# Performance work log

Measured on AMD Instinct MI355X. Metric: run time of the kernel, lower is better.

The kernel has to match this reference:

```python
import jax, jax.numpy as jnp
import numpy as np
from jax import lax

B, C, H, W = 16, 512, 32, 32
CQ = C // 8  # 64
EPS = 1e-5
NEG_SLOPE = 0.2


def _conv1x1(x, Wm, b):
    # x: [B,C,H,W], Wm: [O,C] (1x1 conv kernel squeezed), b: [O]
    return jnp.einsum('oc,bchw->bohw', Wm, x) + b[None, :, None, None]


def _calc_mean_std(feat):
    b, c = feat.shape[:2]
    v = feat.reshape(b, c, -1)
    mean = v.mean(axis=2)[:, :, None, None]
    var = v.var(axis=2, ddof=1) + EPS  # torch .var is unbiased
    std = jnp.sqrt(var)[:, :, None, None]
    return mean, std


def setup_inputs() -> dict:
    key = jax.random.key(0)
    ks = jax.random.split(key, 8)
    s = 0.02
    return {
        'inp': jax.random.normal(ks[0], (B, C, H, W), jnp.float32),
        'x': jax.random.normal(ks[1], (B, C, H, W), jnp.float32),
        'y': jax.random.normal(ks[2], (B, C, H, W), jnp.float32),
        'Wq': jax.random.normal(ks[3], (CQ, C), jnp.float32) * s,
        'bq': jnp.zeros((CQ,), jnp.float32),
        'Wk': jax.random.normal(ks[4], (CQ, C), jnp.float32) * s,
        'bk': jnp.zeros((CQ,), jnp.float32),
        'Wv': jax.random.normal(ks[5], (C, C), jnp.float32) * s,
        'bv': jnp.zeros((C,), jnp.float32),
        'Wc': jax.random.normal(ks[6], (C, 2 * C, 3, 3), jnp.float32) * s,
        'bc': jnp.zeros((C,), jnp.float32),
        'alpha': jnp.ones((1,), jnp.float32),
        'beta': jnp.ones((1,), jnp.float32),
    }


def reference(inp, x, y, Wq, bq, Wk, bk, Wv, bv, Wc, bc, alpha, beta):
    b, c, h, w = x.shape
    n = h * w
    t = float(CQ) ** 0.5  # default temperature sqrt(c_in//8)

    # --- identity-row attention: query from x, key from y ---
    pq = _conv1x1(x, Wq, bq).reshape(b, CQ, n)   # [b,cq,n]
    pk = _conv1x1(y, Wk, bk).reshape(b, CQ, n)
    pv = _conv1x1(x, Wv, bv).reshape(b, c, n)    # [b,c,n]
    attn_iden = jax.nn.softmax(jnp.einsum('bcn,bcm->bnm', pq, pk) / t, axis=-1)

    # --- pose-row attention: query from y, key from x ---
    pq_p = _conv1x1(y, Wq, bq).reshape(b, CQ, n)
    pk_p = _conv1x1(x, Wk, bk).reshape(b, CQ, n)
    attn_pose = jax.nn.softmax(jnp.einsum('bcn,bcm->bnm', pq_p, pk_p) / t, axis=-1)

    # x_update = bmm(value, attn_iden^T): out[c,m] = sum_n pv[c,n]*attn[m,n]
    x_update = jnp.einsum('bcn,bmn->bcm', pv, attn_iden).reshape(b, c, h, w)
    x_update = (1.0 - beta) * x + beta * x_update

    # --- AdaIN: normalize inp, re-affine with x stats ---
    t_mean, t_std = _calc_mean_std(x)
    i_mean, i_std = _calc_mean_std(inp)
    adained = (inp - i_mean) / i_std * t_std + t_mean

    # reverse attention combine with (1 - attn_pose)
    rev = jnp.einsum('bcn,bmn->bcm', adained.reshape(b, c, n), 1.0 - attn_pose)
    rev = rev.reshape(b, c, h, w)
    rev = (1.0 - alpha) * rev + alpha * adained

    # --- conv_comp: 3x3 conv (2C -> C), same padding, LeakyReLU(0.2) ---
    cat = jnp.concatenate([x_update, rev], axis=1)  # [b,2c,h,w]
    out = lax.conv_general_dilated(
        cat, Wc, window_strides=(1, 1), padding='SAME',
        dimension_numbers=('NCHW', 'OIHW', 'NCHW'))
    out = out + bc[None, :, None, None]
    out = jnp.where(out >= 0, out, NEG_SLOPE * out)
    return out
```

## Files before the change

### kernel.cpp

```cpp
#include <hip/hip_runtime.h>

typedef unsigned short u16;
typedef unsigned int u32;

using bf16x8 = __attribute__((ext_vector_type(8))) __bf16;
using f32x4  = __attribute__((ext_vector_type(4))) float;
using u16x4  = __attribute__((ext_vector_type(4))) unsigned short;

__device__ __forceinline__ f32x4 MFMA(bf16x8 a, bf16x8 b, f32x4 c) {
    return __builtin_amdgcn_mfma_f32_16x16x32_bf16(a, b, c, 0, 0, 0);
}

__device__ __forceinline__ u16 f2bf(float f) {
    u32 u = __builtin_bit_cast(u32, f);
    u = (u + 0x7FFFu + ((u >> 16) & 1u)) >> 16;
    return (u16)u;
}
__device__ __forceinline__ float bf2f(u16 h) {
    return __builtin_bit_cast(float, (u32)h << 16);
}

typedef const __attribute__((address_space(1))) unsigned int* gp_t;
typedef __attribute__((address_space(3))) unsigned int* lp_t;

__device__ __forceinline__ void gload16(const void* g, void* l) {
    __builtin_amdgcn_global_load_lds((gp_t)g, (lp_t)l, 16, 0, 0);
}

#define NPADR  1156

static constexpr size_t OFF_XT   = 0;
static constexpr size_t OFF_YT   = OFF_XT  + (size_t)16*1024*512*2;
static constexpr size_t OFF_PJX  = OFF_YT  + (size_t)16*1024*512*2;
static constexpr size_t OFF_PJY  = OFF_PJX + (size_t)16*1024*128*2;
static constexpr size_t OFF_PV   = OFF_PJY + (size_t)16*1024*128*2;
static constexpr size_t OFF_AD   = OFF_PV  + (size_t)16*512*1024*2;
static constexpr size_t OFF_ATTN = OFF_AD  + (size_t)16*512*1024*2;
static constexpr size_t OFF_ATT2 = OFF_ATTN+ (size_t)16*1024*1024*2;
static constexpr size_t OFF_CATT = OFF_ATT2+ (size_t)16*1024*1024*2;
static constexpr size_t OFF_WQK  = OFF_CATT+ (size_t)16*1156*1024*2;
static constexpr size_t OFF_WV   = OFF_WQK + (size_t)128*512*2;
static constexpr size_t OFF_WT   = OFF_WV  + (size_t)512*512*2;
static constexpr size_t OFF_SA   = OFF_WT  + (size_t)9*512*1024*2;
static constexpr size_t OFF_OA   = OFF_SA  + (size_t)16*512*4;
static constexpr size_t OFF_TM   = OFF_OA  + (size_t)16*512*4;

__global__ __launch_bounds__(256) void k_prep_w(const float* __restrict__ Wq,
                                                const float* __restrict__ Wk,
                                                const float* __restrict__ Wv,
                                                u16* __restrict__ wqk, u16* __restrict__ wv) {
    int i = blockIdx.x * 256 + threadIdx.x;
    if (i < 128 * 512) {
        float v = (i < 64 * 512) ? Wq[i] : Wk[i - 64 * 512];
        wqk[i] = f2bf(v);
    }
    if (i < 512 * 512) wv[i] = f2bf(Wv[i]);
}

__global__ __launch_bounds__(256) void k_prep_wt(const float* __restrict__ Wc, u16* __restrict__ wt) {
    int e = blockIdx.x * 256 + threadIdx.x;
    const float* src = Wc + (size_t)e * 9;
#pragma unroll
    for (int tap = 0; tap < 9; tap++) wt[(size_t)tap * 524288 + e] = f2bf(src[tap]);
}

__global__ __launch_bounds__(256) void k_border(u16* __restrict__ catT) {
    int cell = blockIdx.x, b = blockIdx.y;
    int row, col;
    if (cell < 34)       { row = 0;  col = cell; }
    else if (cell < 68)  { row = 33; col = cell - 34; }
    else if (cell < 100) { row = cell - 68 + 1;  col = 0; }
    else                 { row = cell - 100 + 1; col = 33; }
    u16* dst = catT + ((size_t)b * NPADR + row * 34 + col) * 1024;
    u16x4 z = {0, 0, 0, 0};
    ((u16x4*)dst)[threadIdx.x] = z;
}

__global__ __launch_bounds__(256) void k_stats(const float* __restrict__ x, const float* __restrict__ inp,
                                               u16* __restrict__ ad, float* __restrict__ tmA) {
    int row = blockIdx.x;
    int t = threadIdx.x;
    const float4* xr = (const float4*)(x + (size_t)row * 1024);
    const float4* ir = (const float4*)(inp + (size_t)row * 1024);
    float4 a = xr[t], c = ir[t];
    float s1 = a.x + a.y + a.z + a.w;
    float s2 = a.x * a.x + a.y * a.y + a.z * a.z + a.w * a.w;
    float p1 = c.x + c.y + c.z + c.w;
    float p2 = c.x * c.x + c.y * c.y + c.z * c.z + c.w * c.w;
#pragma unroll
    for (int m = 32; m; m >>= 1) {
        s1 += __shfl_xor(s1, m); s2 += __shfl_xor(s2, m);
        p1 += __shfl_xor(p1, m); p2 += __shfl_xor(p2, m);
    }
    __shared__ float red[4][4];
    __shared__ float bcast[2];
    int wv = t >> 6;
    if ((t & 63) == 0) { red[wv][0] = s1; red[wv][1] = s2; red[wv][2] = p1; red[wv][3] = p2; }
    __syncthreads();
    if (t == 0) {
        s1 = red[0][0] + red[1][0] + red[2][0] + red[3][0];
        s2 = red[0][1] + red[1][1] + red[2][1] + red[3][1];
        p1 = red[0][2] + red[1][2] + red[2][2] + red[3][2];
        p2 = red[0][3] + red[1][3] + red[2][3] + red[3][3];
        float tm = s1 * (1.0f / 1024.0f);
        float ts = sqrtf((s2 - 1024.0f * tm * tm) * (1.0f / 1023.0f) + 1e-5f);
        float im = p1 * (1.0f / 1024.0f);
        float is = sqrtf((p2 - 1024.0f * im * im) * (1.0f / 1023.0f) + 1e-5f);
        float sc = ts / is;
        bcast[0] = sc; bcast[1] = tm - im * sc;
        tmA[row] = tm;
    }
    __syncthreads();
    float sc = bcast[0], of = bcast[1];
    u16x4 r;
    r[0] = f2bf(c.x * sc + of); r[1] = f2bf(c.y * sc + of);
    r[2] = f2bf(c.z * sc + of); r[3] = f2bf(c.w * sc + of);
    ((u16x4*)(ad + (size_t)row * 1024))[t] = r;
}

__global__ __launch_bounds__(256) void k_transpose(const float* __restrict__ x, const float* __restrict__ y,
                                                   u16* __restrict__ xT, u16* __restrict__ yT) {
    __shared__ float tile[64][65];
    int b = blockIdx.y;
    int ct = blockIdx.x >> 4;
    int nt = blockIdx.x & 15;
    const float* src = blockIdx.z ? y : x;
    u16* dst = blockIdx.z ? yT : xT;
    int c0 = ct * 64, n0 = nt * 64;
    int ln = threadIdx.x & 63, wv = threadIdx.x >> 6;
#pragma unroll
    for (int i = 0; i < 16; i++) {
        int cl = wv + i * 4;
        tile[cl][ln] = src[((size_t)(b * 512 + c0 + cl)) * 1024 + n0 + ln];
    }
    __syncthreads();
#pragma unroll
    for (int i = 0; i < 16; i++) {
        int nl = wv + i * 4;
        dst[((size_t)(b * 1024 + n0 + nl)) * 512 + c0 + ln] = f2bf(tile[ln][nl]);
    }
}

template <int KTOT, int LDA, int LDB>
__device__ __forceinline__ void gemm128(const u16* __restrict__ Aorig, const u16* __restrict__ Borig,
                                        f32x4 (&acc)[4][4]) {
    __shared__ __align__(16) u16 lds[32768];
    constexpr int NT = KTOT / 32;
    const int tid = threadIdx.x;
    const int l = tid & 63, w = tid >> 6;
    const int lr = l & 15, lg = l >> 4;
    const int moff = (w >> 1) * 64, coff = (w & 1) * 64;
    char* ldsb = (char*)lds;
    auto stage = [&](const u16* orig, int ldx, int bufByte) {
#pragma unroll
        for (int it = 0; it < 2; it++) {
            int slot = it * 256 + tid;
            gload16(orig + (size_t)(slot & 127) * ldx + (slot >> 7) * 8,
                    ldsb + bufByte + it * 4096 + w * 1024);
        }
    };
    auto stageT = [&](int t, int s) {
        stage(Aorig + t * 32, LDA, s * 8192);
        stage(Borig + t * 32, LDB, 32768 + s * 8192);
    };
    stageT(0, 0);
    stageT(1, 1);
    stageT(2, 2);
#pragma unroll 1
    for (int q = 0; q < NT; q++) {
        int qq = q + 3; if (qq >= NT) qq -= NT;
        stageT(qq, (q + 3) & 3);
        asm volatile("s_waitcnt vmcnt(12)" ::: "memory");
        __builtin_amdgcn_s_barrier();
        const char* A = ldsb + (q & 3) * 8192;
        const char* B = ldsb + 32768 + (q & 3) * 8192;
        bf16x8 af[4], bb[4];
#pragma unroll
        for (int i = 0; i < 4; i++) af[i] = *(const bf16x8*)(A + lg * 2048 + (moff + 16 * i + lr) * 16);
#pragma unroll
        for (int i = 0; i < 4; i++) bb[i] = *(const bf16x8*)(B + lg * 2048 + (coff + 16 * i + lr) * 16);
        __builtin_amdgcn_s_setprio(1);
#pragma unroll
        for (int ri = 0; ri < 4; ri++)
#pragma unroll
            for (int ci = 0; ci < 4; ci++) acc[ri][ci] = MFMA(af[ri], bb[ci], acc[ri][ci]);
        __builtin_amdgcn_s_setprio(0);
        __builtin_amdgcn_s_barrier();
    }
    asm volatile("s_waitcnt vmcnt(0)" ::: "memory");
}

__global__ __launch_bounds__(256) void k_proj(const u16* __restrict__ xT, const u16* __restrict__ yT,
                                              const u16* __restrict__ wqk, const float* __restrict__ bq,
                                              const float* __restrict__ bk, u16* __restrict__ pjx,
                                              u16* __restrict__ pjy) {
    int b = blockIdx.y;
    const u16* S = blockIdx.z ? yT : xT;
    u16* D = blockIdx.z ? pjy : pjx;
    int nb = blockIdx.x * 128;
    f32x4 acc[4][4];
#pragma unroll
    for (int i = 0; i < 4; i++)
#pragma unroll
        for (int j = 0; j < 4; j++) acc[i][j] = f32x4{0.f, 0.f, 0.f, 0.f};
    gemm128<512, 512, 512>(S + ((size_t)b * 1024 + nb) * 512, wqk, acc);
    int l = threadIdx.x & 63, w = threadIdx.x >> 6;
    int lr = l & 15, lg = l >> 4;
    int moff = (w >> 1) * 64, coff = (w & 1) * 64;
#pragma unroll
    for (int ri = 0; ri < 4; ri++) {
#pragma unroll
        for (int r = 0; r < 4; r++) {
            int n = nb + moff + 16 * ri + 4 * lg + r;
#pragma unroll
            for (int ci = 0; ci < 4; ci++) {
                int cq = coff + 16 * ci + lr;
                float bias = (cq < 64) ? bq[cq] : bk[cq - 64];
                D[((size_t)b * 1024 + n) * 128 + cq] = f2bf(acc[ri][ci][r] + bias);
            }
        }
    }
}

__global__ __launch_bounds__(256) void k_pv(const u16* __restrict__ xT, const u16* __restrict__ wv,
                                            const float* __restrict__ bv, u16* __restrict__ pv) {
    int b = blockIdx.z;
    int mb = blockIdx.y * 128;
    int nb = blockIdx.x * 128;
    f32x4 acc[4][4];
#pragma unroll
    for (int i = 0; i < 4; i++)
#pragma unroll
        for (int j = 0; j < 4; j++) acc[i][j] = f32x4{0.f, 0.f, 0.f, 0.f};
    gemm128<512, 512, 512>(wv + (size_t)mb * 512, xT + ((size_t)b * 1024 + nb) * 512, acc);
    int l = threadIdx.x & 63, w = threadIdx.x >> 6;
    int lr = l & 15, lg = l >> 4;
    int moff = (w >> 1) * 64, coff = (w & 1) * 64;
#pragma unroll
    for (int ri = 0; ri < 4; ri++) {
#pragma unroll
        for (int r = 0; r < 4; r++) {
            int co = mb + moff + 16 * ri + 4 * lg + r;
            float bias = bv[co];
#pragma unroll
            for (int ci = 0; ci < 4; ci++) {
                int n = nb + coff + 16 * ci + lr;
                pv[((size_t)b * 512 + co) * 1024 + n] = f2bf(acc[ri][ci][r] + bias);
            }
        }
    }
}

__global__ __launch_bounds__(256) void k_score(const u16* __restrict__ pjx, const u16* __restrict__ pjy,
                                               u16* __restrict__ attnA, u16* __restrict__ attnB) {
    const u16* qT = blockIdx.y ? pjy : pjx;
    const u16* kT = blockIdx.y ? pjx : pjy;
    u16* attn = blockIdx.y ? attnB : attnA;
    int g = blockIdx.x * 4 + (threadIdx.x >> 6);
    int b = g >> 6, rb = g & 63;
    int l = threadIdx.x & 63, lr = l & 15, lg = l >> 4;
    int mb = rb * 16;
    const u16* qbase = qT + ((size_t)b * 1024 + mb + lr) * 128 + lg * 8;
    bf16x8 a0 = *(const bf16x8*)(qbase);
    bf16x8 a1 = *(const bf16x8*)(qbase + 32);
    const u16* kbase = kT + ((size_t)b * 1024 + lr) * 128 + 64 + lg * 8;
    f32x4 zero = {0.f, 0.f, 0.f, 0.f};
    float mrun[4] = {-1e30f, -1e30f, -1e30f, -1e30f};
    float srun[4] = {0.f, 0.f, 0.f, 0.f};
    for (int cf = 0; cf < 64; cf++) {
        bf16x8 b0 = *(const bf16x8*)(kbase + (size_t)cf * 16 * 128);
        bf16x8 b1 = *(const bf16x8*)(kbase + (size_t)cf * 16 * 128 + 32);
        f32x4 acc = zero;
        acc = MFMA(a0, b0, acc);
        acc = MFMA(a1, b1, acc);
#pragma unroll
        for (int r = 0; r < 4; r++) {
            float v = acc[r] * 0.125f;
            float mn = fmaxf(mrun[r], v);
            srun[r] = srun[r] * __expf(mrun[r] - mn) + __expf(v - mn);
            mrun[r] = mn;
        }
    }
#pragma unroll
    for (int m = 1; m < 16; m <<= 1) {
#pragma unroll
        for (int r = 0; r < 4; r++) {
            float mo = __shfl_xor(mrun[r], m);
            float so = __shfl_xor(srun[r], m);
            float mn = fmaxf(mrun[r], mo);
            srun[r] = srun[r] * __expf(mrun[r] - mn) + so * __expf(mo - mn);
            mrun[r] = mn;
        }
    }
    float inv[4];
#pragma unroll
    for (int r = 0; r < 4; r++) inv[r] = 1.0f / srun[r];
    for (int cf = 0; cf < 64; cf++) {
        bf16x8 b0 = *(const bf16x8*)(kbase + (size_t)cf * 16 * 128);
        bf16x8 b1 = *(const bf16x8*)(kbase + (size_t)cf * 16 * 128 + 32);
        f32x4 acc = zero;
        acc = MFMA(a0, b0, acc);
        acc = MFMA(a1, b1, acc);
#pragma unroll
        for (int r = 0; r < 4; r++) {
            float v = __expf(acc[r] * 0.125f - mrun[r]) * inv[r];
            attn[((size_t)b * 1024 + mb + 4 * lg + r) * 1024 + cf * 16 + lr] = f2bf(v);
        }
    }
}

__global__ __launch_bounds__(512, 2) void k_value(const u16* __restrict__ attnA, const u16* __restrict__ attnB,
                                                  const u16* __restrict__ pv, const u16* __restrict__ ad,
                                                  const u16* __restrict__ xT, const float* __restrict__ tmA,
                                                  const float* __restrict__ alpha, const float* __restrict__ beta,
                                                  u16* __restrict__ catT) {
    extern __shared__ __align__(16) char dyn[];
    const int id = blockIdx.x;
    const int xcd = id & 7, j = id >> 3;
    const int z = xcd + 8 * (j & 3);
    const int tile = j >> 2;
    const int mbt = tile & 3, cbt = tile >> 2;
    const int b = z & 15, var = z >> 4;
    const u16* Aorig = (var ? attnB : attnA) + ((size_t)b * 1024 + mbt * 256) * 1024;
    const u16* Borig = (var ? ad : pv) + ((size_t)b * 512 + cbt * 256) * 1024;

    const int tid = threadIdx.x;
    const int l = tid & 63, w = tid >> 6;
    const int lr = l & 15, lg = l >> 4;
    const int ow = w >> 1, pw = w & 1;

    auto stageT = [&](int t, int s) {
        char* base = dyn + s * 32768;
#pragma unroll
        for (int it = 0; it < 2; it++) {
            int idx = it * 512 + tid;
            int row = idx & 255, g = idx >> 8;
            gload16(Aorig + (size_t)row * 1024 + t * 32 + g * 8, base + g * 4096 + row * 16);
        }
#pragma unroll
        for (int it = 0; it < 2; it++) {
            int idx = it * 512 + tid;
            int row = idx & 255, g = idx >> 8;
            gload16(Borig + (size_t)row * 1024 + t * 32 + g * 8, base + 16384 + g * 4096 + row * 16);
        }
    };

    f32x4 acc[4][8];
#pragma unroll
    for (int i = 0; i < 4; i++)
#pragma unroll
        for (int jj = 0; jj < 8; jj++) acc[i][jj] = f32x4{0.f, 0.f, 0.f, 0.f};

    stageT(0, 0);
    stageT(1, 1);
#pragma unroll 1
    for (int q = 0; q < 32; q++) {
        int qq = q + 2; if (qq >= 32) qq -= 32;
        stageT(qq, (q + 2) % 3);
        asm volatile("s_waitcnt vmcnt(8)" ::: "memory");
        __builtin_amdgcn_s_barrier();
        const char* A = dyn + (q % 3) * 32768;
        const char* B = A + 16384;
        bf16x8 af[4], bb[8];
#pragma unroll
        for (int i = 0; i < 4; i++) af[i] = *(const bf16x8*)(A + lg * 4096 + (ow * 64 + 16 * i + lr) * 16);
#pragma unroll
        for (int i = 0; i < 8; i++) bb[i] = *(const bf16x8*)(B + lg * 4096 + (pw * 128 + 16 * i + lr) * 16);
        __builtin_amdgcn_s_setprio(1);
#pragma unroll
        for (int ri = 0; ri < 4; ri++)
#pragma unroll
            for (int ci = 0; ci < 8; ci++) acc[ri][ci] = MFMA(af[ri], bb[ci], acc[ri][ci]);
        __builtin_amdgcn_s_setprio(0);
        __builtin_amdgcn_s_barrier();
    }
    asm volatile("s_waitcnt vmcnt(0)" ::: "memory");

    float sc = var ? alpha[0] : beta[0];
#pragma unroll
    for (int ri = 0; ri < 4; ri++) {
#pragma unroll
        for (int r = 0; r < 4; r++) {
            int m = mbt * 256 + ow * 64 + 16 * ri + 4 * lg + r;
            int pidx = ((m >> 5) + 1) * 34 + (m & 31) + 1;
#pragma unroll
            for (int ci = 0; ci < 8; ci++) {
                int c = cbt * 256 + pw * 128 + 16 * ci + lr;
                float av = acc[ri][ci][r];
                float res;
                if (var == 0) {
                    float xv = bf2f(xT[((size_t)b * 1024 + m) * 512 + c]);
                    res = (1.f - sc) * xv + sc * av;
                } else {
                    float tm = tmA[b * 512 + c];
                    float adv = bf2f(ad[((size_t)b * 512 + c) * 1024 + m]);
                    res = (1.f - sc) * (1024.f * tm - av) + sc * adv;
                }
                catT[((size_t)b * NPADR + pidx) * 1024 + (var ? 512 : 0) + c] = f2bf(res);
            }
        }
    }
}

__global__ __launch_bounds__(512, 2) void k_conv(const u16* __restrict__ wt, const u16* __restrict__ catT,
                                                 const float* __restrict__ bc, float* __restrict__ out) {
    extern __shared__ __align__(16) char dyn[];
    const int id = blockIdx.x;
    const int xcd = id & 7, j = id >> 3;
    const int obt = j & 3;
    const int pbb = xcd + 8 * (j >> 2);
    const int pbt = pbb & 3, b = pbb >> 2;

    const int tid = threadIdx.x;
    const int l = tid & 63, w = tid >> 6;
    const int lr = l & 15, lg = l >> 4;
    const int ob = obt * 128;
    const int pb = pbt * 256;
    const int r0 = pbt * 8;
    const int ow = w >> 2, pw = w & 3;
    const u16* catB = catT + (size_t)b * NPADR * 1024 + (size_t)r0 * 34 * 1024;

    auto stageA = [&](int tap, int ck, int slot) {
        char* base = dyn + slot * 8192;
        int row = tid & 127, g = tid >> 7;
        gload16(wt + ((size_t)tap * 512 + ob + row) * 1024 + ck + g * 8,
                base + g * 2048 + row * 16);
    };
    auto stageB = [&](int ck, int sel) {
        char* base = dyn + 24576 + sel * 24576;
#pragma unroll
        for (int it = 0; it < 3; it++) {
            int idx = it * 512 + tid;
            int g = idx / 384;
            int row = idx - g * 384;
            gload16(catB + (size_t)row * 1024 + ck + g * 8,
                    base + g * 6144 + row * 16);
        }
    };

    int aoff[4], rbase[4];
#pragma unroll
    for (int i = 0; i < 4; i++) {
        aoff[i] = lg * 2048 + (ow * 64 + 16 * i + lr) * 16;
        int p = pw * 64 + 16 * i + lr;
        rbase[i] = ((p >> 5) + 1) * 34 + (p & 31) + 1;
    }

    f32x4 acc[4][4];
#pragma unroll
    for (int i = 0; i < 4; i++)
#pragma unroll
        for (int jj = 0; jj < 4; jj++) acc[i][jj] = f32x4{0.f, 0.f, 0.f, 0.f};

    stageA(0, 0, 0);
    stageB(0, 0);
    stageA(1, 0, 1);
    int phase = 0;
#pragma unroll 1
    for (int ckI = 0; ckI < 32; ckI++) {
#pragma unroll
        for (int tap = 0; tap < 9; tap++, phase++) {
            {
                int t2 = tap + 2;
                int c2 = ckI + (t2 >= 9);
                if (t2 >= 9) t2 -= 9;
                if (c2 >= 32) c2 = 0;
                stageA(t2, c2 * 32, (phase + 2) % 3);
            }
            if (tap == 5) {
                int cn = ckI + 1;
                stageB((cn >= 32 ? 0 : cn) * 32, cn & 1);
            }
            if (tap >= 5 && tap <= 7) asm volatile("s_waitcnt vmcnt(5)" ::: "memory");
            else                      asm volatile("s_waitcnt vmcnt(2)" ::: "memory");
            __builtin_amdgcn_s_barrier();
            const char* A = dyn + (phase % 3) * 8192;
            const char* B = dyn + 24576 + (ckI & 1) * 24576;
            const int drow = (tap / 3 - 1) * 34 + (tap % 3 - 1);
            bf16x8 af[4], bb[4];
#pragma unroll
            for (int i = 0; i < 4; i++) af[i] = *(const bf16x8*)(A + aoff[i]);
#pragma unroll
            for (int i = 0; i < 4; i++) bb[i] = *(const bf16x8*)(B + lg * 6144 + (rbase[i] + drow) * 16);
            __builtin_amdgcn_s_setprio(1);
#pragma unroll
            for (int ri = 0; ri < 4; ri++)
#pragma unroll
                for (int ci = 0; ci < 4; ci++) acc[ri][ci] = MFMA(af[ri], bb[ci], acc[ri][ci]);
            __builtin_amdgcn_s_setprio(0);
            __builtin_amdgcn_s_barrier();
        }
    }
    asm volatile("s_waitcnt vmcnt(0)" ::: "memory");
#pragma unroll
    for (int ri = 0; ri < 4; ri++) {
#pragma unroll
        for (int r = 0; r < 4; r++) {
            int o = ob + ow * 64 + 16 * ri + 4 * lg + r;
            float bias = bc[o];
#pragma unroll
            for (int ci = 0; ci < 4; ci++) {
                int p = pb + pw * 64 + 16 * ci + lr;
                float v = acc[ri][ci][r] + bias;
                v = (v >= 0.f) ? v : 0.2f * v;
                out[((size_t)b * 512 + o) * 1024 + p] = v;
            }
        }
    }
}

extern "C" void kernel_launch(void* const* d_in, const int* in_sizes, int n_in,
                              void* d_out, int out_size, void* d_ws, size_t ws_size,
                              hipStream_t stream) {
    (void)in_sizes; (void)n_in; (void)out_size; (void)ws_size;
    const float* inp = (const float*)d_in[0];
    const float* x   = (const float*)d_in[1];
    const float* y   = (const float*)d_in[2];
    const float* Wq  = (const float*)d_in[3];
    const float* bq  = (const float*)d_in[4];
    const float* Wk  = (const float*)d_in[5];
    const float* bk  = (const float*)d_in[6];
    const float* Wv  = (const float*)d_in[7];
    const float* bv  = (const float*)d_in[8];
    const float* Wc  = (const float*)d_in[9];
    const float* bc  = (const float*)d_in[10];
    const float* alpha = (const float*)d_in[11];
    const float* beta  = (const float*)d_in[12];
    float* out = (float*)d_out;

    char* ws = (char*)d_ws;
    u16* xT   = (u16*)(ws + OFF_XT);
    u16* yT   = (u16*)(ws + OFF_YT);
    u16* pjx  = (u16*)(ws + OFF_PJX);
    u16* pjy  = (u16*)(ws + OFF_PJY);
    u16* pv   = (u16*)(ws + OFF_PV);
    u16* ad   = (u16*)(ws + OFF_AD);
    u16* attnA = (u16*)(ws + OFF_ATTN);
    u16* attnB = (u16*)(ws + OFF_ATT2);
    u16* catT = (u16*)(ws + OFF_CATT);
    u16* wqk  = (u16*)(ws + OFF_WQK);
    u16* wv   = (u16*)(ws + OFF_WV);
    u16* wt   = (u16*)(ws + OFF_WT);
    float* tmA = (float*)(ws + OFF_TM);

    hipFuncSetAttribute((const void*)k_conv,  hipFuncAttributeMaxDynamicSharedMemorySize, 73728);
    hipFuncSetAttribute((const void*)k_value, hipFuncAttributeMaxDynamicSharedMemorySize, 98304);

    k_prep_w<<<1024, 256, 0, stream>>>(Wq, Wk, Wv, wqk, wv);
    k_prep_wt<<<2048, 256, 0, stream>>>(Wc, wt);
    k_border<<<dim3(132, 16), 256, 0, stream>>>(catT);
    k_stats<<<8192, 256, 0, stream>>>(x, inp, ad, tmA);
    k_transpose<<<dim3(128, 16, 2), 256, 0, stream>>>(x, y, xT, yT);
    k_proj<<<dim3(8, 16, 2), 256, 0, stream>>>(xT, yT, wqk, bq, bk, pjx, pjy);
    k_pv<<<dim3(8, 4, 16), 256, 0, stream>>>(xT, wv, bv, pv);
    k_score<<<dim3(256, 2), 256, 0, stream>>>(pjx, pjy, attnA, attnB);
    k_value<<<256, 512, 98304, stream>>>(attnA, attnB, pv, ad, xT, tmA, alpha, beta, catT);
    k_conv<<<256, 512, 73728, stream>>>(wt, catT, bc, out);
}
```

Measured before the change: 378.6 us.

## Load conv weight fragments directly into registers and drop per-tap barriers

The 3x3 conv kernel no longer stages weight tiles through shared memory with a triple buffer. Each lane now loads its A-operand fragments straight from global memory into registers, prefetching the next tap while the current one computes. Barriers are only issued once per channel chunk instead of twice per tap, and shared memory drops to the double-buffered activation tile. The trade-off is that global weight reads are duplicated across the four pixel-wave groups and are less coalesced, and more registers are held for the prefetch.

```diff
diff --git a/kernel.cpp b/kernel.cpp
--- a/kernel.cpp
+++ b/kernel.cpp
@@ -420,14 +420,8 @@
     const int ow = w >> 2, pw = w & 3;
     const u16* catB = catT + (size_t)b * NPADR * 1024 + (size_t)r0 * 34 * 1024;
 
-    auto stageA = [&](int tap, int ck, int slot) {
-        char* base = dyn + slot * 8192;
-        int row = tid & 127, g = tid >> 7;
-        gload16(wt + ((size_t)tap * 512 + ob + row) * 1024 + ck + g * 8,
-                base + g * 2048 + row * 16);
-    };
     auto stageB = [&](int ck, int sel) {
-        char* base = dyn + 24576 + sel * 24576;
+        char* base = dyn + sel * 24576;
 #pragma unroll
         for (int it = 0; it < 3; it++) {
             int idx = it * 512 + tid;
@@ -438,10 +432,11 @@
         }
     };
 
-    int aoff[4], rbase[4];
+    const u16* wbase = wt + ((size_t)(ob + ow * 64 + lr)) * 1024 + lg * 8;
+
+    int rbase[4];
 #pragma unroll
     for (int i = 0; i < 4; i++) {
-        aoff[i] = lg * 2048 + (ow * 64 + 16 * i + lr) * 16;
         int p = pw * 64 + 16 * i + lr;
         rbase[i] = ((p >> 5) + 1) * 34 + (p & 31) + 1;
     }
@@ -452,43 +447,43 @@
 #pragma unroll
         for (int jj = 0; jj < 4; jj++) acc[i][jj] = f32x4{0.f, 0.f, 0.f, 0.f};
 
-    stageA(0, 0, 0);
+    bf16x8 afc[4], afn[4];
     stageB(0, 0);
-    stageA(1, 0, 1);
-    int phase = 0;
+#pragma unroll
+    for (int i = 0; i < 4; i++) afc[i] = *(const bf16x8*)(wbase + (size_t)i * 16384);
+
 #pragma unroll 1
     for (int ckI = 0; ckI < 32; ckI++) {
 #pragma unroll
-        for (int tap = 0; tap < 9; tap++, phase++) {
-            {
-                int t2 = tap + 2;
-                int c2 = ckI + (t2 >= 9);
-                if (t2 >= 9) t2 -= 9;
-                if (c2 >= 32) c2 = 0;
-                stageA(t2, c2 * 32, (phase + 2) % 3);
+        for (int tap = 0; tap < 9; tap++) {
+            if (tap == 0) {
+                asm volatile("s_waitcnt vmcnt(4)" ::: "memory");
+                __builtin_amdgcn_s_barrier();
             }
             if (tap == 5) {
                 int cn = ckI + 1;
                 stageB((cn >= 32 ? 0 : cn) * 32, cn & 1);
             }
-            if (tap >= 5 && tap <= 7) asm volatile("s_waitcnt vmcnt(5)" ::: "memory");
-            else                      asm volatile("s_waitcnt vmcnt(2)" ::: "memory");
-            __builtin_amdgcn_s_barrier();
-            const char* A = dyn + (phase % 3) * 8192;
-            const char* B = dyn + 24576 + (ckI & 1) * 24576;
+            {
+                int nt = tap + 1, nc = ckI;
+                if (nt == 9) { nt = 0; nc = ckI + 1; if (nc == 32) nc = 0; }
+                const u16* ap = wbase + (size_t)nt * 524288 + nc * 32;
+#pragma unroll
+                for (int i = 0; i < 4; i++) afn[i] = *(const bf16x8*)(ap + (size_t)i * 16384);
+            }
+            const char* B = dyn + (ckI & 1) * 24576;
             const int drow = (tap / 3 - 1) * 34 + (tap % 3 - 1);
-            bf16x8 af[4], bb[4];
-#pragma unroll
-            for (int i = 0; i < 4; i++) af[i] = *(const bf16x8*)(A + aoff[i]);
+            bf16x8 bb[4];
 #pragma unroll
             for (int i = 0; i < 4; i++) bb[i] = *(const bf16x8*)(B + lg * 6144 + (rbase[i] + drow) * 16);
             __builtin_amdgcn_s_setprio(1);
 #pragma unroll
             for (int ri = 0; ri < 4; ri++)
 #pragma unroll
-                for (int ci = 0; ci < 4; ci++) acc[ri][ci] = MFMA(af[ri], bb[ci], acc[ri][ci]);
+                for (int ci = 0; ci < 4; ci++) acc[ri][ci] = MFMA(afc[ri], bb[ci], acc[ri][ci]);
             __builtin_amdgcn_s_setprio(0);
-            __builtin_amdgcn_s_barrier();
+#pragma unroll
+            for (int i = 0; i < 4; i++) afc[i] = afn[i];
         }
     }
     asm volatile("s_waitcnt vmcnt(0)" ::: "memory");
@@ -543,7 +538,7 @@
     u16* wt   = (u16*)(ws + OFF_WT);
     float* tmA = (float*)(ws + OFF_TM);
 
-    hipFuncSetAttribute((const void*)k_conv,  hipFuncAttributeMaxDynamicSharedMemorySize, 73728);
+    hipFuncSetAttribute((const void*)k_conv,  hipFuncAttributeMaxDynamicSharedMemorySize, 49152);
     hipFuncSetAttribute((const void*)k_value, hipFuncAttributeMaxDynamicSharedMemorySize, 98304);
 
     k_prep_w<<<1024, 256, 0, stream>>>(Wq, Wk, Wv, wqk, wv);
@@ -555,5 +550,5 @@
     k_pv<<<dim3(8, 4, 16), 256, 0, stream>>>(xT, wv, bv, pv);
     k_score<<<dim3(256, 2), 256, 0, stream>>>(pjx, pjy, attnA, attnB);
     k_value<<<256, 512, 98304, stream>>>(attnA, attnB, pv, ad, xT, tmA, alpha, beta, catT);
-    k_conv<<<256, 512, 73728, stream>>>(wt, catT, bc, out);
-}
+    k_conv<<<256, 512, 49152, stream>>>(wt, catT, bc, out);
+}
```

Result: slower. 521.0 us (+37.6%).
